# Kernel optimization log

Measured on AMD Instinct MI355X. Metric: run time of the kernel, lower is better.

The kernel has to match this reference:

```python
import jax, jax.numpy as jnp
import numpy as np


def setup_inputs() -> dict:
    key = jax.random.key(0)
    k1, k2 = jax.random.split(key)
    B, C, H, W = 1, 32, 128, 256
    feaL = jax.random.normal(k1, (B, C, H, W), dtype=jnp.float32)
    feaR = jax.random.normal(k2, (B, C, H, W), dtype=jnp.float32)
    return {"feaL": feaL, "feaR": feaR, "min_disp": 0, "max_disp": 128}


def _cost_volume_and_softargmax(feaL, feaR, min_disp, max_disp):
    # Faithful to GCNet.cost_volume (i >= 0 branch; min_disp = 0) followed by
    # GCNet.softargmax over the disparity axis. Note the source assigns feaR
    # into BOTH channel halves for i >= 0; feaL is not used in the volume.
    B, C, H, W = feaL.shape
    md = max_disp // 2
    mn = min_disp // 2
    d = jnp.arange(mn, md)                      # [D] disparity indices
    w = jnp.arange(W)                           # [W]
    valid = (w[None, :] >= d[:, None])          # [D, W], zeros where w < d

    # first half: cost[:, 0:C, i, :, i:] = feaR[:, :, :, i:]
    left = feaR[:, :, None, :, :] * valid[None, None, :, None, :]  # [B,C,D,H,W]

    # second half: cost[:, C:, i, :, i:] = feaR[:, :, :, :W-i]  (shift right by d)
    idx = jnp.clip(w[None, :] - d[:, None], 0, W - 1)              # [D, W]
    shifted = feaR[:, :, :, idx]                                    # [B,C,H,D,W]
    shifted = jnp.transpose(shifted, (0, 1, 3, 2, 4))               # [B,C,D,H,W]
    right = shifted * valid[None, None, :, None, :]

    cost = jnp.concatenate([left, right], axis=1)                   # [B,2C,D,H,W]

    # softargmax over disparity axis (dim=2)
    p = jax.nn.softmax(cost, axis=2)
    vec = d.astype(cost.dtype)[None, None, :, None, None]
    disp = jnp.sum(p * vec, axis=2)                                  # [B,2C,H,W]
    return disp


def reference(feaL, feaR, min_disp, max_disp):
    return _cost_volume_and_softargmax(feaL, feaR, min_disp, max_disp)
```

## Files before the change

kernel.cpp:

```cpp
#include <hip/hip_runtime.h>


#define CC 32
#define HH 128
#define WW 256

__global__ __launch_bounds__(256) void gcnet_kernel(const float* __restrict__ feaR,
                                                    float* __restrict__ out) {
    const int w    = threadIdx.x;
    const int lane = w & 63;
    const int wid  = w >> 6;

    __shared__ float sP[WW];
    __shared__ float sQ[WW];
    __shared__ float wPs[4];
    __shared__ float wQs[4];

    for (int r = blockIdx.x; r < CC * HH; r += gridDim.x) {
        const int c = r >> 7;
        const int h = r & 127;

        const float v = feaR[(size_t)r * WW + w];
        const float e = __expf(v);

        float p = e;
        float q = e * (float)w;
        #pragma unroll
        for (int off = 1; off < 64; off <<= 1) {
            float pu = __shfl_up(p, off, 64);
            float qu = __shfl_up(q, off, 64);
            if (lane >= off) { p += pu; q += qu; }
        }
        if (lane == 63) { wPs[wid] = p; wQs[wid] = q; }
        __syncthreads();
        #pragma unroll
        for (int j = 0; j < 3; ++j) {
            if (wid > j) { p += wPs[j]; q += wQs[j]; }
        }
        sP[w] = p;
        sQ[w] = q;
        __syncthreads();

        float dP = p - (w >= 64 ? sP[w - 64] : 0.0f);
        float dQ = q - (w >= 64 ? sQ[w - 64] : 0.0f);
        float num = (float)w * dP - dQ;
        float den = dP;
        if (w < 63) {
            float S1 = 0.5f * (float)w * (float)(w + 1);
            num += 2016.0f - S1;
            den += (float)(63 - w);
        }
        out[((size_t)(CC + c) * HH + h) * WW + w] = num / den;

        float n1  = (w >= 63) ? 64.0f : (float)(w + 1);
        float S1l = 0.5f * n1 * (n1 - 1.0f);
        float n0  = 64.0f - n1;
        float S0l = 2016.0f - S1l;
        out[((size_t)c * HH + h) * WW + w] = (S1l * e + S0l) / (n1 * e + n0);

        __syncthreads();
    }
}

extern "C" void kernel_launch(void* const* d_in, const int* in_sizes, int n_in,
                              void* d_out, int out_size, void* d_ws, size_t ws_size,
                              hipStream_t stream) {
    const float* feaR = (const float*)d_in[1];
    float* out = (float*)d_out;
    dim3 grid(CC * HH);
    dim3 block(WW);
    gcnet_kernel<<<grid, block, 0, stream>>>(feaR, out);
}
```

Measured before the change: 10.79 us.

## Map one row per wavefront with float4 loads and shuffle-only prefix scan

Each 64-lane wavefront now handles a whole 256-element row, with each lane loading four consecutive values as a float4. The row prefix sums are built from a per-lane serial scan plus a wavefront shuffle scan, so the LDS arrays and __syncthreads barriers go away. The shifted-by-64 difference is taken with a cross-lane shuffle, and outputs are written as float4. The grid shrinks fourfold, with four rows per block. This removes block-level synchronization and shared-memory traffic and widens memory accesses, at the cost of more registers per lane.

```diff
diff --git a/kernel.cpp b/kernel.cpp
--- a/kernel.cpp
+++ b/kernel.cpp
@@ -7,59 +7,83 @@
 
 __global__ __launch_bounds__(256) void gcnet_kernel(const float* __restrict__ feaR,
                                                     float* __restrict__ out) {
-    const int w    = threadIdx.x;
-    const int lane = w & 63;
-    const int wid  = w >> 6;
+    const int t   = threadIdx.x & 63;
+    const int wid = threadIdx.x >> 6;
+    const int r   = (blockIdx.x << 2) + wid;
+    const int c   = r >> 7;
+    const int h   = r & 127;
 
-    __shared__ float sP[WW];
-    __shared__ float sQ[WW];
-    __shared__ float wPs[4];
-    __shared__ float wQs[4];
+    const float4 v = *reinterpret_cast<const float4*>(feaR + ((size_t)r << 8) + (t << 2));
 
-    for (int r = blockIdx.x; r < CC * HH; r += gridDim.x) {
-        const int c = r >> 7;
-        const int h = r & 127;
+    const float e0 = __expf(v.x);
+    const float e1 = __expf(v.y);
+    const float e2 = __expf(v.z);
+    const float e3 = __expf(v.w);
 
-        const float v = feaR[(size_t)r * WW + w];
-        const float e = __expf(v);
+    const float w0 = (float)(t << 2);
 
-        float p = e;
-        float q = e * (float)w;
+    const float p0 = e0, p1 = p0 + e1, p2 = p1 + e2, p3 = p2 + e3;
+    const float q0 = e0 * w0;
+    const float q1 = q0 + e1 * (w0 + 1.0f);
+    const float q2 = q1 + e2 * (w0 + 2.0f);
+    const float q3 = q2 + e3 * (w0 + 3.0f);
+
+    float sp = p3, sq = q3;
+    #pragma unroll
+    for (int off = 1; off < 64; off <<= 1) {
+        float a = __shfl_up(sp, off, 64);
+        float b = __shfl_up(sq, off, 64);
+        if (t >= off) { sp += a; sq += b; }
+    }
+    const float offP = sp - p3;
+    const float offQ = sq - q3;
+
+    const float P0 = offP + p0, P1 = offP + p1, P2 = offP + p2, P3 = offP + p3;
+    const float Q0 = offQ + q0, Q1 = offQ + q1, Q2 = offQ + q2, Q3 = offQ + q3;
+
+    const int src = (t - 16) & 63;
+    const float Pm0 = __shfl(P0, src, 64), Pm1 = __shfl(P1, src, 64);
+    const float Pm2 = __shfl(P2, src, 64), Pm3 = __shfl(P3, src, 64);
+    const float Qm0 = __shfl(Q0, src, 64), Qm1 = __shfl(Q1, src, 64);
+    const float Qm2 = __shfl(Q2, src, 64), Qm3 = __shfl(Q3, src, 64);
+
+    const bool hi = (t >= 16);
+
+    float4 right, left;
+    {
+        float P[4]  = {P0, P1, P2, P3};
+        float Q[4]  = {Q0, Q1, Q2, Q3};
+        float PM[4] = {Pm0, Pm1, Pm2, Pm3};
+        float QM[4] = {Qm0, Qm1, Qm2, Qm3};
+        float E[4]  = {e0, e1, e2, e3};
+        float R[4], L[4];
         #pragma unroll
-        for (int off = 1; off < 64; off <<= 1) {
-            float pu = __shfl_up(p, off, 64);
-            float qu = __shfl_up(q, off, 64);
-            if (lane >= off) { p += pu; q += qu; }
+        for (int j = 0; j < 4; ++j) {
+            const float wj = w0 + (float)j;
+            float dP = P[j] - (hi ? PM[j] : 0.0f);
+            float dQ = Q[j] - (hi ? QM[j] : 0.0f);
+            float num = wj * dP - dQ;
+            float den = dP;
+            if (wj < 63.0f) {
+                float S1 = 0.5f * wj * (wj + 1.0f);
+                num += 2016.0f - S1;
+                den += 63.0f - wj;
+            }
+            R[j] = num / den;
+            float n1  = fminf(wj + 1.0f, 64.0f);
+            float S1l = 0.5f * n1 * (n1 - 1.0f);
+            float n0  = 64.0f - n1;
+            float S0l = 2016.0f - S1l;
+            L[j] = (S1l * E[j] + S0l) / (n1 * E[j] + n0);
         }
-        if (lane == 63) { wPs[wid] = p; wQs[wid] = q; }
-        __syncthreads();
-        #pragma unroll
-        for (int j = 0; j < 3; ++j) {
-            if (wid > j) { p += wPs[j]; q += wQs[j]; }
-        }
-        sP[w] = p;
-        sQ[w] = q;
-        __syncthreads();
+        right = make_float4(R[0], R[1], R[2], R[3]);
+        left  = make_float4(L[0], L[1], L[2], L[3]);
+    }
 
-        float dP = p - (w >= 64 ? sP[w - 64] : 0.0f);
-        float dQ = q - (w >= 64 ? sQ[w - 64] : 0.0f);
-        float num = (float)w * dP - dQ;
-        float den = dP;
-        if (w < 63) {
-            float S1 = 0.5f * (float)w * (float)(w + 1);
-            num += 2016.0f - S1;
-            den += (float)(63 - w);
-        }
-        out[((size_t)(CC + c) * HH + h) * WW + w] = num / den;
-
-        float n1  = (w >= 63) ? 64.0f : (float)(w + 1);
-        float S1l = 0.5f * n1 * (n1 - 1.0f);
-        float n0  = 64.0f - n1;
-        float S0l = 2016.0f - S1l;
-        out[((size_t)c * HH + h) * WW + w] = (S1l * e + S0l) / (n1 * e + n0);
-
-        __syncthreads();
-    }
+    float* outR = out + (((size_t)(CC + c) * HH + h) << 8) + (t << 2);
+    float* outL = out + (((size_t)c * HH + h) << 8) + (t << 2);
+    *reinterpret_cast<float4*>(outR) = right;
+    *reinterpret_cast<float4*>(outL) = left;
 }
 
 extern "C" void kernel_launch(void* const* d_in, const int* in_sizes, int n_in,
@@ -67,7 +91,7 @@
                               hipStream_t stream) {
     const float* feaR = (const float*)d_in[1];
     float* out = (float*)d_out;
-    dim3 grid(CC * HH);
-    dim3 block(WW);
+    dim3 grid((CC * HH) / 4);
+    dim3 block(256);
     gcnet_kernel<<<grid, block, 0, stream>>>(feaR, out);
 }
```

New measurement: 10.50 us. 2.7% less time.
